# Kernel tuning notes

Measured on AMD Instinct MI355X. Metric: run time of the kernel, lower is better.

The kernel has to match this reference:

```python
import jax, jax.numpy as jnp
import numpy as np

B, N, F_IN, D = 32, 100, 10, 64
TAU = 10.0
ALPHA = 0.2  # GAT leaky-relu slope
EPS = 1e-8


def _cosine_sim(e):
    n = e / (jnp.linalg.norm(e, axis=-1, keepdims=True) + EPS)
    return n @ n.T


def _gumbel_softmax_hard(key, logits, tau):
    u = jax.random.uniform(key, logits.shape, minval=1e-20, maxval=1.0)
    g = -jnp.log(-jnp.log(u))
    y = jax.nn.softmax((logits + g) / tau, axis=-1)
    y_hard = jax.nn.one_hot(jnp.argmax(y, axis=-1), logits.shape[-1], dtype=y.dtype)
    # straight-through
    return y_hard + y - jax.lax.stop_gradient(y)


def _gat(x, adj, emb, W, b, a):
    # single GAT layer; attention keys are embedding-augmented features
    h = x @ W + b                       # (Nt, D)
    k = h + emb                         # (Nt, D)
    d = h.shape[-1]
    e = jax.nn.leaky_relu((k @ a[:d])[:, None] + (k @ a[d:])[None, :], ALPHA)  # (Nt, Nt)
    e = jnp.where(adj > 0, e, jnp.asarray(-9e15, e.dtype))
    att = jax.nn.softmax(e, axis=-1)
    hp = att @ h
    return jax.nn.elu(hp), att


def setup_inputs():
    key = jax.random.key(0)
    ks = jax.random.split(key, 12)
    s = 0.1
    return {
        "data": jax.random.normal(ks[0], (B, N, F_IN), jnp.float32),
        "node_emb": jax.random.normal(ks[1], (N, D), jnp.float32),
        "lin_W": jax.random.normal(ks[2], (F_IN, D), jnp.float32) * s,
        "lin_b": jnp.zeros((D,), jnp.float32),
        "gat_s_W": jax.random.normal(ks[3], (F_IN, D), jnp.float32) * s,
        "gat_s_b": jnp.zeros((D,), jnp.float32),
        "gat_s_a": jax.random.normal(ks[4], (2 * D,), jnp.float32) * s,
        "gat_d_W": jax.random.normal(ks[5], (F_IN, D), jnp.float32) * s,
        "gat_d_b": jnp.zeros((D,), jnp.float32),
        "gat_d_a": jax.random.normal(ks[6], (2 * D,), jnp.float32) * s,
        "bn_gamma": jnp.ones((D,), jnp.float32),
        "bn_beta": jnp.zeros((D,), jnp.float32),
        "out_W": jax.random.normal(ks[7], (D, 1), jnp.float32) * s,
        "out_b": jnp.zeros((1,), jnp.float32),
    }


def reference(data, node_emb, lin_W, lin_b, gat_s_W, gat_s_b, gat_s_a,
              gat_d_W, gat_d_b, gat_d_a, bn_gamma, bn_beta, out_W, out_b):
    k1, k2 = jax.random.split(jax.random.key(42))
    Nt = B * N
    x = data.reshape(Nt, F_IN)
    # block-diagonal mask: edges only within each batch sample
    blk = jnp.arange(Nt) // N
    mask = (blk[:, None] == blk[None, :]).astype(x.dtype)

    # --- static graph from node embeddings ---
    sim_s = _cosine_sim(node_emb)                       # (N, N)
    adj_s = _gumbel_softmax_hard(k1, jnp.stack([sim_s, 1.0 - sim_s], -1), TAU)[..., 0]
    adj_s = ((adj_s + jnp.eye(N, dtype=adj_s.dtype)) > 0).astype(x.dtype)  # bool->float (kills grad, as torch)
    adj_s = jnp.tile(adj_s, (B, B)) * mask              # (Nt, Nt)

    # --- dynamic graph from current features ---
    emb_d = x @ lin_W + lin_b                           # (Nt, D)
    sim_d = _cosine_sim(emb_d)                          # (Nt, Nt)
    adj_d = _gumbel_softmax_hard(k2, jnp.stack([sim_d, 1.0 - sim_d], -1), TAU)[..., 0]
    adj_d = adj_d * mask

    emb_rep = jnp.tile(node_emb, (B, 1))                # (Nt, D)
    emb_S, _ = _gat(x, adj_s, emb_rep, gat_s_W, gat_s_b, gat_s_a)
    emb_D, _ = _gat(x, adj_d, emb_rep, gat_d_W, gat_d_b, gat_d_a)
    emb = emb_S + 0.01 * emb_D                          # (Nt, D)

    out = emb.reshape(B, N, D) * node_emb               # (B, N, D)
    # BatchNorm1d over channel D (training-mode batch stats), then ReLU
    m = out.mean(axis=(0, 1))
    v = out.var(axis=(0, 1))
    out = (out - m) / jnp.sqrt(v + 1e-5) * bn_gamma + bn_beta
    out = jax.nn.relu(out)
    # dropout p=0.2 is identity in eval mode
    out = out @ out_W + out_b                           # (B, N, 1)
    return out.reshape(-1, N)                           # (B, N)
```

## Files before the change

kernel.cpp:

```cpp
#include <hip/hip_runtime.h>
#include <cstdint>

#define NT 3200
#define NN 100
#define FD 10
#define DD 64

__host__ __device__ inline void tf2x32(uint32_t ks0, uint32_t ks1, uint32_t x0,
                                       uint32_t x1, uint32_t& o0, uint32_t& o1) {
  uint32_t ks2 = ks0 ^ ks1 ^ 0x1BD11BDAu;
  x0 += ks0; x1 += ks1;
#define TF_RND(r) { x0 += x1; x1 = (x1 << (r)) | (x1 >> (32 - (r))); x1 ^= x0; }
  TF_RND(13) TF_RND(15) TF_RND(26) TF_RND(6)
  x0 += ks1; x1 += ks2 + 1u;
  TF_RND(17) TF_RND(29) TF_RND(16) TF_RND(24)
  x0 += ks2; x1 += ks0 + 2u;
  TF_RND(13) TF_RND(15) TF_RND(26) TF_RND(6)
  x0 += ks0; x1 += ks1 + 3u;
  TF_RND(17) TF_RND(29) TF_RND(16) TF_RND(24)
  x0 += ks1; x1 += ks2 + 4u;
  TF_RND(13) TF_RND(15) TF_RND(26) TF_RND(6)
  x0 += ks2; x1 += ks0 + 5u;
#undef TF_RND
  o0 = x0; o1 = x1;
}

__device__ inline float gumbel_noise(uint32_t ka, uint32_t kb, uint32_t cnt) {
  uint32_t o0, o1;
  tf2x32(ka, kb, 0u, cnt, o0, o1);
  uint32_t bits = o0 ^ o1;
  float u = __uint_as_float((bits >> 9) | 0x3F800000u) - 1.0f;
  u = fmaxf(u, 1e-20f);
  return -logf(-logf(u));
}

__global__ __launch_bounds__(64) void k_prep(
    const float* __restrict__ x, const float* __restrict__ ne,
    const float* __restrict__ lW, const float* __restrict__ lb,
    const float* __restrict__ Ws, const float* __restrict__ bs,
    const float* __restrict__ as_, const float* __restrict__ Wd,
    const float* __restrict__ bd, const float* __restrict__ ad,
    float* __restrict__ h_s, float* __restrict__ h_d, float* __restrict__ nd,
    float* __restrict__ q_s, float* __restrict__ kk_s, float* __restrict__ q_d,
    float* __restrict__ kk_d) {
  int i = blockIdx.x;
  int ch = threadIdx.x;
  const float* xr = x + i * FD;
  float hs = bs[ch], hd = bd[ch], ed = lb[ch];
#pragma unroll
  for (int f = 0; f < FD; ++f) {
    float xv = xr[f];
    hs = fmaf(xv, Ws[f * DD + ch], hs);
    hd = fmaf(xv, Wd[f * DD + ch], hd);
    ed = fmaf(xv, lW[f * DD + ch], ed);
  }
  h_s[i * DD + ch] = hs;
  h_d[i * DD + ch] = hd;
  float ss = ed * ed;
  for (int off = 32; off > 0; off >>= 1) ss += __shfl_xor(ss, off, 64);
  nd[i * DD + ch] = ed / (sqrtf(ss) + 1e-8f);
  int r = i % NN;
  float em = ne[r * DD + ch];
  float ks = hs + em, kd = hd + em;
  float qs = ks * as_[ch], kks = ks * as_[DD + ch];
  float qd = kd * ad[ch], kkd = kd * ad[DD + ch];
  for (int off = 32; off > 0; off >>= 1) {
    qs += __shfl_xor(qs, off, 64);
    kks += __shfl_xor(kks, off, 64);
    qd += __shfl_xor(qd, off, 64);
    kkd += __shfl_xor(kkd, off, 64);
  }
  if (ch == 0) { q_s[i] = qs; kk_s[i] = kks; q_d[i] = qd; kk_d[i] = kkd; }
}

__global__ void k_adjs(const float* __restrict__ ne, float* __restrict__ adjS,
                       uint32_t k1a, uint32_t k1b) {
  int p = blockIdx.x * 256 + threadIdx.x;
  if (p >= NN * NN) return;
  int r = p / NN, c = p - r * NN;
  const float* er = ne + r * DD;
  const float* ec = ne + c * DD;
  float sr = 0.0f, sc = 0.0f;
#pragma unroll
  for (int k = 0; k < DD; ++k) {
    sr = fmaf(er[k], er[k], sr);
    sc = fmaf(ec[k], ec[k], sc);
  }
  float dr = sqrtf(sr) + 1e-8f, dc = sqrtf(sc) + 1e-8f;
  float sim = 0.0f;
#pragma unroll
  for (int k = 0; k < DD; ++k) sim = fmaf(er[k] / dr, ec[k] / dc, sim);
  float g0 = gumbel_noise(k1a, k1b, (uint32_t)(2 * p));
  float g1 = gumbel_noise(k1a, k1b, (uint32_t)(2 * p + 1));
  bool edge = (sim + g0 >= 1.0f - sim + g1) || (r == c);
  adjS[p] = edge ? 1.0f : 0.0f;
}

__global__ __launch_bounds__(128) void k_attn(
    const float* __restrict__ h_s, const float* __restrict__ h_d,
    const float* __restrict__ nd, const float* __restrict__ q_s,
    const float* __restrict__ kk_s, const float* __restrict__ q_d,
    const float* __restrict__ kk_d, const float* __restrict__ adjS,
    const float* __restrict__ ne, float* __restrict__ o, uint32_t k2a,
    uint32_t k2b) {
  __shared__ float lnd[NN * 65];
  __shared__ float red[128];
  __shared__ float att_s[NN];
  __shared__ float att_d[NN];
  int i = blockIdx.x;
  int tid = threadIdx.x;
  int b = i / NN, r = i - b * NN;
  int base = b * NN;
  for (int idx = tid; idx < NN * DD; idx += 128) {
    int row = idx >> 6, ch = idx & 63;
    lnd[row * 65 + ch] = nd[(base + row) * DD + ch];
  }
  __syncthreads();
  float es = -9e15f, ed = -9e15f;
  if (tid < NN) {
    int j = base + tid;
    if (adjS[r * NN + tid] > 0.0f) {
      float v = q_s[i] + kk_s[j];
      es = (v >= 0.0f) ? v : 0.2f * v;
    }
    float sim = 0.0f;
    const float* ni = &lnd[r * 65];
    const float* nj = &lnd[tid * 65];
#pragma unroll
    for (int k = 0; k < DD; ++k) sim = fmaf(ni[k], nj[k], sim);
    uint32_t cnt = ((uint32_t)i * 3200u + (uint32_t)j) * 2u;
    float g0 = gumbel_noise(k2a, k2b, cnt);
    float g1 = gumbel_noise(k2a, k2b, cnt + 1u);
    if (sim + g0 >= 1.0f - sim + g1) {
      float v = q_d[i] + kk_d[j];
      ed = (v >= 0.0f) ? v : 0.2f * v;
    }
  }
  red[tid] = es;
  __syncthreads();
  for (int s = 64; s > 0; s >>= 1) {
    if (tid < s) red[tid] = fmaxf(red[tid], red[tid + s]);
    __syncthreads();
  }
  float ms = red[0];
  __syncthreads();
  float wv = (tid < NN) ? expf(es - ms) : 0.0f;
  red[tid] = wv;
  __syncthreads();
  for (int s = 64; s > 0; s >>= 1) {
    if (tid < s) red[tid] += red[tid + s];
    __syncthreads();
  }
  float Ss = red[0];
  __syncthreads();
  if (tid < NN) att_s[tid] = wv / Ss;
  red[tid] = ed;
  __syncthreads();
  for (int s = 64; s > 0; s >>= 1) {
    if (tid < s) red[tid] = fmaxf(red[tid], red[tid + s]);
    __syncthreads();
  }
  float md = red[0];
  __syncthreads();
  float wd = (tid < NN) ? expf(ed - md) : 0.0f;
  red[tid] = wd;
  __syncthreads();
  for (int s = 64; s > 0; s >>= 1) {
    if (tid < s) red[tid] += red[tid + s];
    __syncthreads();
  }
  float Sd = red[0];
  __syncthreads();
  if (tid < NN) att_d[tid] = wd / Sd;
  __syncthreads();
  if (tid < DD) {
    int ch = tid;
    float hs = 0.0f, hd2 = 0.0f;
    for (int c = 0; c < NN; ++c) {
      hs = fmaf(att_s[c], h_s[(base + c) * DD + ch], hs);
      hd2 = fmaf(att_d[c], h_d[(base + c) * DD + ch], hd2);
    }
    float eS = (hs > 0.0f) ? hs : expm1f(hs);
    float eD = (hd2 > 0.0f) ? hd2 : expm1f(hd2);
    float emb = eS + 0.01f * eD;
    o[i * DD + ch] = emb * ne[r * DD + ch];
  }
}

__global__ void k_bn(const float* __restrict__ o, const float* __restrict__ gamma,
                     float* __restrict__ mean, float* __restrict__ scale) {
  int ch = blockIdx.x;
  int tid = threadIdx.x;
  __shared__ float red[256];
  float s = 0.0f;
  for (int row = tid; row < NT; row += 256) s += o[row * DD + ch];
  red[tid] = s;
  __syncthreads();
  for (int k = 128; k > 0; k >>= 1) {
    if (tid < k) red[tid] += red[tid + k];
    __syncthreads();
  }
  float m = red[0] / (float)NT;
  __syncthreads();
  float v = 0.0f;
  for (int row = tid; row < NT; row += 256) {
    float d = o[row * DD + ch] - m;
    v = fmaf(d, d, v);
  }
  red[tid] = v;
  __syncthreads();
  for (int k = 128; k > 0; k >>= 1) {
    if (tid < k) red[tid] += red[tid + k];
    __syncthreads();
  }
  if (tid == 0) {
    float var = red[0] / (float)NT;
    mean[ch] = m;
    scale[ch] = gamma[ch] / sqrtf(var + 1e-5f);
  }
}

__global__ void k_final(const float* __restrict__ o, const float* __restrict__ mean,
                        const float* __restrict__ scale,
                        const float* __restrict__ beta,
                        const float* __restrict__ outW,
                        const float* __restrict__ outb, float* __restrict__ out) {
  int lane = threadIdx.x & 63;
  int i = blockIdx.x * 4 + (threadIdx.x >> 6);
  float x = o[i * DD + lane];
  float v = (x - mean[lane]) * scale[lane] + beta[lane];
  v = fmaxf(v, 0.0f);
  float p = v * outW[lane];
  for (int off = 32; off > 0; off >>= 1) p += __shfl_xor(p, off, 64);
  if (lane == 0) out[i] = p + outb[0];
}

extern "C" void kernel_launch(void* const* d_in, const int* in_sizes, int n_in,
                              void* d_out, int out_size, void* d_ws,
                              size_t ws_size, hipStream_t stream) {
  const float* data = (const float*)d_in[0];
  const float* node_emb = (const float*)d_in[1];
  const float* lin_W = (const float*)d_in[2];
  const float* lin_b = (const float*)d_in[3];
  const float* gat_s_W = (const float*)d_in[4];
  const float* gat_s_b = (const float*)d_in[5];
  const float* gat_s_a = (const float*)d_in[6];
  const float* gat_d_W = (const float*)d_in[7];
  const float* gat_d_b = (const float*)d_in[8];
  const float* gat_d_a = (const float*)d_in[9];
  const float* bn_gamma = (const float*)d_in[10];
  const float* bn_beta = (const float*)d_in[11];
  const float* out_W = (const float*)d_in[12];
  const float* out_b = (const float*)d_in[13];
  float* out = (float*)d_out;

  float* ws = (float*)d_ws;
  float* h_s = ws;
  float* h_d = ws + 204800;
  float* nd = ws + 409600;
  float* q_s = ws + 614400;
  float* kk_s = ws + 617600;
  float* q_d = ws + 620800;
  float* kk_d = ws + 624000;
  float* adjS = ws + 627200;
  float* o = ws + 637200;
  float* mean = ws + 842000;
  float* scale = ws + 842064;

  uint32_t k1a, k1b, k2a, k2b;
  tf2x32(0u, 42u, 0u, 0u, k1a, k1b);
  tf2x32(0u, 42u, 0u, 1u, k2a, k2b);

  k_prep<<<NT, 64, 0, stream>>>(data, node_emb, lin_W, lin_b, gat_s_W, gat_s_b,
                                gat_s_a, gat_d_W, gat_d_b, gat_d_a, h_s, h_d, nd,
                                q_s, kk_s, q_d, kk_d);
  k_adjs<<<(NN * NN + 255) / 256, 256, 0, stream>>>(node_emb, adjS, k1a, k1b);
  k_attn<<<NT, 128, 0, stream>>>(h_s, h_d, nd, q_s, kk_s, q_d, kk_d, adjS,
                                 node_emb, o, k2a, k2b);
  k_bn<<<DD, 256, 0, stream>>>(o, bn_gamma, mean, scale);
  k_final<<<NT / 4, 256, 0, stream>>>(o, mean, scale, bn_beta, out_W, out_b, out);
}
```

Before: 148.0 us.

## Fuse prep with static adjacency, warp-per-row attention, and atomic BN statistics

Merges the feature projection kernel and the static-graph adjacency kernel into a single launch. The adjacency path now stages node embeddings in shared memory and normalizes them once per block. The attention kernel is restructured so that each wave handles one row, using wave shuffles for the softmax reductions in place of block-level shared-memory tree reductions, and each block now processes four rows instead of one. The separate batchnorm statistics kernel is removed: per-channel sum and sum-of-squares are accumulated with atomics in the attention kernel and consumed in the final kernel. This cuts launches, barriers and a full pass over the output. The costs are float atomics, which make the accumulation order nondeterministic, an extra memset, and a variance computed as E[x^2]-m^2, which is less numerically stable.

```diff
diff --git a/kernel.cpp b/kernel.cpp
--- a/kernel.cpp
+++ b/kernel.cpp
@@ -34,7 +34,7 @@
   return -logf(-logf(u));
 }
 
-__global__ __launch_bounds__(64) void k_prep(
+__global__ __launch_bounds__(256) void k_prep_adj(
     const float* __restrict__ x, const float* __restrict__ ne,
     const float* __restrict__ lW, const float* __restrict__ lb,
     const float* __restrict__ Ws, const float* __restrict__ bs,
@@ -42,193 +42,184 @@
     const float* __restrict__ bd, const float* __restrict__ ad,
     float* __restrict__ h_s, float* __restrict__ h_d, float* __restrict__ nd,
     float* __restrict__ q_s, float* __restrict__ kk_s, float* __restrict__ q_d,
-    float* __restrict__ kk_d) {
-  int i = blockIdx.x;
-  int ch = threadIdx.x;
-  const float* xr = x + i * FD;
-  float hs = bs[ch], hd = bd[ch], ed = lb[ch];
+    float* __restrict__ kk_d, float* __restrict__ adjS, uint32_t k1a,
+    uint32_t k1b) {
+  __shared__ float sne[NN * 65];
+  __shared__ float dnorm[NN];
+  int tid = threadIdx.x, wid = tid >> 6, lane = tid & 63;
+  int blk = blockIdx.x;
+  if (blk < 800) {
+    int i = blk * 4 + wid;
+    const float* xr = x + i * FD;
+    float hs = bs[lane], hd = bd[lane], ed = lb[lane];
 #pragma unroll
-  for (int f = 0; f < FD; ++f) {
-    float xv = xr[f];
-    hs = fmaf(xv, Ws[f * DD + ch], hs);
-    hd = fmaf(xv, Wd[f * DD + ch], hd);
-    ed = fmaf(xv, lW[f * DD + ch], ed);
-  }
-  h_s[i * DD + ch] = hs;
-  h_d[i * DD + ch] = hd;
-  float ss = ed * ed;
-  for (int off = 32; off > 0; off >>= 1) ss += __shfl_xor(ss, off, 64);
-  nd[i * DD + ch] = ed / (sqrtf(ss) + 1e-8f);
-  int r = i % NN;
-  float em = ne[r * DD + ch];
-  float ks = hs + em, kd = hd + em;
-  float qs = ks * as_[ch], kks = ks * as_[DD + ch];
-  float qd = kd * ad[ch], kkd = kd * ad[DD + ch];
-  for (int off = 32; off > 0; off >>= 1) {
-    qs += __shfl_xor(qs, off, 64);
-    kks += __shfl_xor(kks, off, 64);
-    qd += __shfl_xor(qd, off, 64);
-    kkd += __shfl_xor(kkd, off, 64);
-  }
-  if (ch == 0) { q_s[i] = qs; kk_s[i] = kks; q_d[i] = qd; kk_d[i] = kkd; }
-}
-
-__global__ void k_adjs(const float* __restrict__ ne, float* __restrict__ adjS,
-                       uint32_t k1a, uint32_t k1b) {
-  int p = blockIdx.x * 256 + threadIdx.x;
-  if (p >= NN * NN) return;
-  int r = p / NN, c = p - r * NN;
-  const float* er = ne + r * DD;
-  const float* ec = ne + c * DD;
-  float sr = 0.0f, sc = 0.0f;
+    for (int f = 0; f < FD; ++f) {
+      float xv = xr[f];
+      hs = fmaf(xv, Ws[f * DD + lane], hs);
+      hd = fmaf(xv, Wd[f * DD + lane], hd);
+      ed = fmaf(xv, lW[f * DD + lane], ed);
+    }
+    h_s[i * DD + lane] = hs;
+    h_d[i * DD + lane] = hd;
+    float ss = ed * ed;
+    for (int off = 32; off > 0; off >>= 1) ss += __shfl_xor(ss, off, 64);
+    nd[i * DD + lane] = ed / (sqrtf(ss) + 1e-8f);
+    int r = i % NN;
+    float em = ne[r * DD + lane];
+    float ks = hs + em, kd = hd + em;
+    float qs = ks * as_[lane], kks = ks * as_[DD + lane];
+    float qd = kd * ad[lane], kkd = kd * ad[DD + lane];
+    for (int off = 32; off > 0; off >>= 1) {
+      qs += __shfl_xor(qs, off, 64);
+      kks += __shfl_xor(kks, off, 64);
+      qd += __shfl_xor(qd, off, 64);
+      kkd += __shfl_xor(kkd, off, 64);
+    }
+    if (lane == 0) { q_s[i] = qs; kk_s[i] = kks; q_d[i] = qd; kk_d[i] = kkd; }
+  } else {
+    for (int idx = tid; idx < NN * DD; idx += 256)
+      sne[(idx >> 6) * 65 + (idx & 63)] = ne[idx];
+    __syncthreads();
+    for (int row = wid; row < NN; row += 4) {
+      float v = sne[row * 65 + lane];
+      float ss = v * v;
+      for (int off = 32; off > 0; off >>= 1) ss += __shfl_xor(ss, off, 64);
+      if (lane == 0) dnorm[row] = sqrtf(ss) + 1e-8f;
+    }
+    __syncthreads();
+    for (int idx = tid; idx < NN * DD; idx += 256) {
+      int row = idx >> 6;
+      sne[row * 65 + (idx & 63)] /= dnorm[row];
+    }
+    __syncthreads();
+    int p = (blk - 800) * 256 + tid;
+    if (p < NN * NN) {
+      int r = p / NN, c = p - r * NN;
+      float sim = 0.0f;
 #pragma unroll
-  for (int k = 0; k < DD; ++k) {
-    sr = fmaf(er[k], er[k], sr);
-    sc = fmaf(ec[k], ec[k], sc);
-  }
-  float dr = sqrtf(sr) + 1e-8f, dc = sqrtf(sc) + 1e-8f;
-  float sim = 0.0f;
-#pragma unroll
-  for (int k = 0; k < DD; ++k) sim = fmaf(er[k] / dr, ec[k] / dc, sim);
-  float g0 = gumbel_noise(k1a, k1b, (uint32_t)(2 * p));
-  float g1 = gumbel_noise(k1a, k1b, (uint32_t)(2 * p + 1));
-  bool edge = (sim + g0 >= 1.0f - sim + g1) || (r == c);
-  adjS[p] = edge ? 1.0f : 0.0f;
-}
-
-__global__ __launch_bounds__(128) void k_attn(
+      for (int k = 0; k < DD; ++k)
+        sim = fmaf(sne[r * 65 + k], sne[c * 65 + k], sim);
+      float g0 = gumbel_noise(k1a, k1b, (uint32_t)(2 * p));
+      float g1 = gumbel_noise(k1a, k1b, (uint32_t)(2 * p + 1));
+      bool edge = (sim + g0 >= 1.0f - sim + g1) || (r == c);
+      adjS[p] = edge ? 1.0f : 0.0f;
+    }
+  }
+}
+
+__global__ __launch_bounds__(256) void k_attn(
     const float* __restrict__ h_s, const float* __restrict__ h_d,
     const float* __restrict__ nd, const float* __restrict__ q_s,
     const float* __restrict__ kk_s, const float* __restrict__ q_d,
     const float* __restrict__ kk_d, const float* __restrict__ adjS,
-    const float* __restrict__ ne, float* __restrict__ o, uint32_t k2a,
-    uint32_t k2b) {
+    const float* __restrict__ ne, float* __restrict__ o,
+    float* __restrict__ gstat, uint32_t k2a, uint32_t k2b) {
   __shared__ float lnd[NN * 65];
-  __shared__ float red[128];
-  __shared__ float att_s[NN];
-  __shared__ float att_d[NN];
-  int i = blockIdx.x;
-  int tid = threadIdx.x;
-  int b = i / NN, r = i - b * NN;
+  __shared__ float att[4][2][NN];
+  int tid = threadIdx.x, wid = tid >> 6, lane = tid & 63;
+  int blk = blockIdx.x;
+  int b = blk / 25, rb = (blk % 25) * 4;
   int base = b * NN;
-  for (int idx = tid; idx < NN * DD; idx += 128) {
-    int row = idx >> 6, ch = idx & 63;
-    lnd[row * 65 + ch] = nd[(base + row) * DD + ch];
-  }
+  for (int idx = tid; idx < NN * DD; idx += 256)
+    lnd[(idx >> 6) * 65 + (idx & 63)] = nd[base * DD + idx];
   __syncthreads();
-  float es = -9e15f, ed = -9e15f;
-  if (tid < NN) {
-    int j = base + tid;
-    if (adjS[r * NN + tid] > 0.0f) {
-      float v = q_s[i] + kk_s[j];
-      es = (v >= 0.0f) ? v : 0.2f * v;
-    }
-    float sim = 0.0f;
-    const float* ni = &lnd[r * 65];
-    const float* nj = &lnd[tid * 65];
+
+  int r = rb + wid;
+  int i = base + r;
+  float sqs = q_s[i], sqd = q_d[i];
+  int j0 = lane, j1 = lane + 64;
+  bool v1 = (j1 < NN);
+  int jj1 = v1 ? j1 : 0;
+  float sim0 = 0.0f, sim1 = 0.0f;
+  const float* ndr = &lnd[r * 65];
+  const float* nj0 = &lnd[j0 * 65];
+  const float* nj1 = &lnd[jj1 * 65];
 #pragma unroll
-    for (int k = 0; k < DD; ++k) sim = fmaf(ni[k], nj[k], sim);
-    uint32_t cnt = ((uint32_t)i * 3200u + (uint32_t)j) * 2u;
-    float g0 = gumbel_noise(k2a, k2b, cnt);
-    float g1 = gumbel_noise(k2a, k2b, cnt + 1u);
-    if (sim + g0 >= 1.0f - sim + g1) {
-      float v = q_d[i] + kk_d[j];
-      ed = (v >= 0.0f) ? v : 0.2f * v;
-    }
-  }
-  red[tid] = es;
+  for (int k = 0; k < DD; ++k) {
+    float a = ndr[k];
+    sim0 = fmaf(a, nj0[k], sim0);
+    sim1 = fmaf(a, nj1[k], sim1);
+  }
+  float es0 = -9e15f, es1 = -9e15f, ed0 = -9e15f, ed1 = -9e15f;
+  if (adjS[r * NN + j0] > 0.0f) {
+    float v = sqs + kk_s[base + j0];
+    es0 = (v >= 0.0f) ? v : 0.2f * v;
+  }
+  if (v1 && adjS[r * NN + j1] > 0.0f) {
+    float v = sqs + kk_s[base + j1];
+    es1 = (v >= 0.0f) ? v : 0.2f * v;
+  }
+  {
+    uint32_t c0 = ((uint32_t)i * 3200u + (uint32_t)(base + j0)) * 2u;
+    float g0 = gumbel_noise(k2a, k2b, c0);
+    float g1 = gumbel_noise(k2a, k2b, c0 + 1u);
+    if (sim0 + g0 >= 1.0f - sim0 + g1) {
+      float v = sqd + kk_d[base + j0];
+      ed0 = (v >= 0.0f) ? v : 0.2f * v;
+    }
+  }
+  if (v1) {
+    uint32_t c1 = ((uint32_t)i * 3200u + (uint32_t)(base + j1)) * 2u;
+    float g0 = gumbel_noise(k2a, k2b, c1);
+    float g1 = gumbel_noise(k2a, k2b, c1 + 1u);
+    if (sim1 + g0 >= 1.0f - sim1 + g1) {
+      float v = sqd + kk_d[base + j1];
+      ed1 = (v >= 0.0f) ? v : 0.2f * v;
+    }
+  }
+  float ms = fmaxf(es0, es1);
+  for (int off = 32; off > 0; off >>= 1) ms = fmaxf(ms, __shfl_xor(ms, off, 64));
+  float ws0 = expf(es0 - ms);
+  float ws1 = v1 ? expf(es1 - ms) : 0.0f;
+  float Ss = ws0 + ws1;
+  for (int off = 32; off > 0; off >>= 1) Ss += __shfl_xor(Ss, off, 64);
+  att[wid][0][j0] = ws0 / Ss;
+  if (v1) att[wid][0][j1] = ws1 / Ss;
+  float md = fmaxf(ed0, ed1);
+  for (int off = 32; off > 0; off >>= 1) md = fmaxf(md, __shfl_xor(md, off, 64));
+  float wd0 = expf(ed0 - md);
+  float wd1 = v1 ? expf(ed1 - md) : 0.0f;
+  float Sd = wd0 + wd1;
+  for (int off = 32; off > 0; off >>= 1) Sd += __shfl_xor(Sd, off, 64);
+  att[wid][1][j0] = wd0 / Sd;
+  if (v1) att[wid][1][j1] = wd1 / Sd;
+  float hs = 0.0f, hd2 = 0.0f;
+  const float* hsp = h_s + base * DD + lane;
+  const float* hdp = h_d + base * DD + lane;
+#pragma unroll 4
+  for (int j = 0; j < NN; ++j) {
+    hs = fmaf(att[wid][0][j], hsp[j * DD], hs);
+    hd2 = fmaf(att[wid][1][j], hdp[j * DD], hd2);
+  }
+  float eS = (hs > 0.0f) ? hs : expm1f(hs);
+  float eD = (hd2 > 0.0f) ? hd2 : expm1f(hd2);
+  float ov = (eS + 0.01f * eD) * ne[r * DD + lane];
+  o[i * DD + lane] = ov;
+  att[wid][0][lane] = ov;
+  att[wid][1][lane] = ov * ov;
   __syncthreads();
-  for (int s = 64; s > 0; s >>= 1) {
-    if (tid < s) red[tid] = fmaxf(red[tid], red[tid + s]);
-    __syncthreads();
-  }
-  float ms = red[0];
-  __syncthreads();
-  float wv = (tid < NN) ? expf(es - ms) : 0.0f;
-  red[tid] = wv;
-  __syncthreads();
-  for (int s = 64; s > 0; s >>= 1) {
-    if (tid < s) red[tid] += red[tid + s];
-    __syncthreads();
-  }
-  float Ss = red[0];
-  __syncthreads();
-  if (tid < NN) att_s[tid] = wv / Ss;
-  red[tid] = ed;
-  __syncthreads();
-  for (int s = 64; s > 0; s >>= 1) {
-    if (tid < s) red[tid] = fmaxf(red[tid], red[tid + s]);
-    __syncthreads();
-  }
-  float md = red[0];
-  __syncthreads();
-  float wd = (tid < NN) ? expf(ed - md) : 0.0f;
-  red[tid] = wd;
-  __syncthreads();
-  for (int s = 64; s > 0; s >>= 1) {
-    if (tid < s) red[tid] += red[tid + s];
-    __syncthreads();
-  }
-  float Sd = red[0];
-  __syncthreads();
-  if (tid < NN) att_d[tid] = wd / Sd;
-  __syncthreads();
-  if (tid < DD) {
-    int ch = tid;
-    float hs = 0.0f, hd2 = 0.0f;
-    for (int c = 0; c < NN; ++c) {
-      hs = fmaf(att_s[c], h_s[(base + c) * DD + ch], hs);
-      hd2 = fmaf(att_d[c], h_d[(base + c) * DD + ch], hd2);
-    }
-    float eS = (hs > 0.0f) ? hs : expm1f(hs);
-    float eD = (hd2 > 0.0f) ? hd2 : expm1f(hd2);
-    float emb = eS + 0.01f * eD;
-    o[i * DD + ch] = emb * ne[r * DD + ch];
-  }
-}
-
-__global__ void k_bn(const float* __restrict__ o, const float* __restrict__ gamma,
-                     float* __restrict__ mean, float* __restrict__ scale) {
-  int ch = blockIdx.x;
-  int tid = threadIdx.x;
-  __shared__ float red[256];
-  float s = 0.0f;
-  for (int row = tid; row < NT; row += 256) s += o[row * DD + ch];
-  red[tid] = s;
-  __syncthreads();
-  for (int k = 128; k > 0; k >>= 1) {
-    if (tid < k) red[tid] += red[tid + k];
-    __syncthreads();
-  }
-  float m = red[0] / (float)NT;
-  __syncthreads();
-  float v = 0.0f;
-  for (int row = tid; row < NT; row += 256) {
-    float d = o[row * DD + ch] - m;
-    v = fmaf(d, d, v);
-  }
-  red[tid] = v;
-  __syncthreads();
-  for (int k = 128; k > 0; k >>= 1) {
-    if (tid < k) red[tid] += red[tid + k];
-    __syncthreads();
-  }
-  if (tid == 0) {
-    float var = red[0] / (float)NT;
-    mean[ch] = m;
-    scale[ch] = gamma[ch] / sqrtf(var + 1e-5f);
-  }
-}
-
-__global__ void k_final(const float* __restrict__ o, const float* __restrict__ mean,
-                        const float* __restrict__ scale,
-                        const float* __restrict__ beta,
-                        const float* __restrict__ outW,
-                        const float* __restrict__ outb, float* __restrict__ out) {
-  int lane = threadIdx.x & 63;
-  int i = blockIdx.x * 4 + (threadIdx.x >> 6);
-  float x = o[i * DD + lane];
-  float v = (x - mean[lane]) * scale[lane] + beta[lane];
+  if (wid == 0) {
+    float s = att[0][0][lane] + att[1][0][lane] + att[2][0][lane] + att[3][0][lane];
+    unsafeAtomicAdd(&gstat[lane], s);
+  } else if (wid == 1) {
+    float s = att[0][1][lane] + att[1][1][lane] + att[2][1][lane] + att[3][1][lane];
+    unsafeAtomicAdd(&gstat[64 + lane], s);
+  }
+}
+
+__global__ __launch_bounds__(256) void k_final(
+    const float* __restrict__ o, const float* __restrict__ gstat,
+    const float* __restrict__ gamma, const float* __restrict__ beta,
+    const float* __restrict__ outW, const float* __restrict__ outb,
+    float* __restrict__ out) {
+  int tid = threadIdx.x, wid = tid >> 6, lane = tid & 63;
+  int i = blockIdx.x * 4 + wid;
+  float m = gstat[lane] * (1.0f / NT);
+  float ex2 = gstat[64 + lane] * (1.0f / NT);
+  float var = ex2 - m * m;
+  float scale = gamma[lane] / sqrtf(var + 1e-5f);
+  float xv = o[i * DD + lane];
+  float v = (xv - m) * scale + beta[lane];
   v = fmaxf(v, 0.0f);
   float p = v * outW[lane];
   for (int off = 32; off > 0; off >>= 1) p += __shfl_xor(p, off, 64);
@@ -264,19 +255,19 @@
   float* kk_d = ws + 624000;
   float* adjS = ws + 627200;
   float* o = ws + 637200;
-  float* mean = ws + 842000;
-  float* scale = ws + 842064;
+  float* gstat = ws + 842000;
 
   uint32_t k1a, k1b, k2a, k2b;
   tf2x32(0u, 42u, 0u, 0u, k1a, k1b);
   tf2x32(0u, 42u, 0u, 1u, k2a, k2b);
 
-  k_prep<<<NT, 64, 0, stream>>>(data, node_emb, lin_W, lin_b, gat_s_W, gat_s_b,
-                                gat_s_a, gat_d_W, gat_d_b, gat_d_a, h_s, h_d, nd,
-                                q_s, kk_s, q_d, kk_d);
-  k_adjs<<<(NN * NN + 255) / 256, 256, 0, stream>>>(node_emb, adjS, k1a, k1b);
-  k_attn<<<NT, 128, 0, stream>>>(h_s, h_d, nd, q_s, kk_s, q_d, kk_d, adjS,
-                                 node_emb, o, k2a, k2b);
-  k_bn<<<DD, 256, 0, stream>>>(o, bn_gamma, mean, scale);
-  k_final<<<NT / 4, 256, 0, stream>>>(o, mean, scale, bn_beta, out_W, out_b, out);
-}
+  hipMemsetAsync(gstat, 0, 128 * sizeof(float), stream);
+  k_prep_adj<<<840, 256, 0, stream>>>(data, node_emb, lin_W, lin_b, gat_s_W,
+                                      gat_s_b, gat_s_a, gat_d_W, gat_d_b,
+                                      gat_d_a, h_s, h_d, nd, q_s, kk_s, q_d,
+                                      kk_d, adjS, k1a, k1b);
+  k_attn<<<800, 256, 0, stream>>>(h_s, h_d, nd, q_s, kk_s, q_d, kk_d, adjS,
+                                  node_emb, o, gstat, k2a, k2b);
+  k_final<<<800, 256, 0, stream>>>(o, gstat, bn_gamma, bn_beta, out_W, out_b,
+                                   out);
+}
```

After: 137.3 us. 7.2% less time.
